# Optimization experiments

Measured on AMD Instinct MI355X. Metric: run time of the kernel, lower is better.

## Reference

```python
import jax, jax.numpy as jnp
from jax import lax
import numpy as np

STRIDE = 16
A = 9  # num anchors per location
PRE_NMS = 6000
POST_NMS = 300
NMS_THRESH = 0.7
MIN_SIZE = 16.0


def _generate_anchors(base_size=16, ratios=(0.5, 1.0, 2.0), scales=(8, 16, 32)):
    ratios = np.array(ratios, dtype=np.float64)
    scales = np.array(scales, dtype=np.float64)
    base = np.array([0, 0, base_size - 1, base_size - 1], dtype=np.float64)
    w = base[2] - base[0] + 1
    h = base[3] - base[1] + 1
    xc = base[0] + 0.5 * (w - 1)
    yc = base[1] + 0.5 * (h - 1)
    size = w * h
    ws = np.round(np.sqrt(size / ratios))
    hs = np.round(ws * ratios)
    def mk(ws, hs):
        return np.stack([xc - 0.5 * (ws - 1), yc - 0.5 * (hs - 1),
                         xc + 0.5 * (ws - 1), yc + 0.5 * (hs - 1)], axis=1)
    ratio_anchors = mk(ws, hs)  # (3,4)
    out = []
    for ra in ratio_anchors:
        rw = ra[2] - ra[0] + 1
        rh = ra[3] - ra[1] + 1
        out.append(mk(rw * scales, rh * scales))
    return np.concatenate(out, axis=0).astype(np.float32)  # (9,4)


def _conv(x, w, b, padding):
    y = lax.conv_general_dilated(x, w, (1, 1), padding,
                                 dimension_numbers=('NCHW', 'OIHW', 'NCHW'))
    return y + b[None, :, None, None]


def _rpn_forward(feature_map, im_info, conv_w, conv_b, cls_w, cls_b, bbox_w, bbox_b):
    H, W = feature_map.shape[2], feature_map.shape[3]
    x = jax.nn.relu(_conv(feature_map, conv_w, conv_b, 'SAME'))
    cls_score = _conv(x, cls_w, cls_b, 'VALID')      # [1, 2A, H, W]
    bbox_pred = _conv(x, bbox_w, bbox_b, 'VALID')    # [1, 4A, H, W]

    # softmax over the 2 classes: view (1, 2, A, H, W)
    prob = jax.nn.softmax(cls_score.reshape(1, 2, A, H, W), axis=1).reshape(1, 2 * A, H, W)
    fg_scores = prob[:, A:, :, :].transpose(0, 2, 3, 1).reshape(-1)     # [H*W*A]
    deltas = bbox_pred.transpose(0, 2, 3, 1).reshape(-1, 4)             # [H*W*A, 4]

    # anchors shifted over the grid (K, A, 4) -> (K*A, 4), x varies fastest
    base_anchors = jnp.asarray(_generate_anchors())
    shift_x = jnp.arange(W, dtype=jnp.float32) * STRIDE
    shift_y = jnp.arange(H, dtype=jnp.float32) * STRIDE
    sx, sy = jnp.meshgrid(shift_x, shift_y)  # (H, W)
    shifts = jnp.stack([sx.ravel(), sy.ravel(), sx.ravel(), sy.ravel()], axis=1)
    anchors = (base_anchors[None, :, :] + shifts[:, None, :]).reshape(-1, 4)

    # bbox_transform_inv
    aw = anchors[:, 2] - anchors[:, 0] + 1.0
    ah = anchors[:, 3] - anchors[:, 1] + 1.0
    ax = anchors[:, 0] + 0.5 * aw
    ay = anchors[:, 1] + 0.5 * ah
    dx, dy, dw, dh = deltas[:, 0], deltas[:, 1], deltas[:, 2], deltas[:, 3]
    px = dx * aw + ax
    py = dy * ah + ay
    pw = jnp.exp(dw) * aw
    ph = jnp.exp(dh) * ah
    x1 = px - 0.5 * pw
    y1 = py - 0.5 * ph
    x2 = px + 0.5 * pw
    y2 = py + 0.5 * ph

    # clip to image
    x1 = jnp.clip(x1, 0.0, im_info[1] - 1.0)
    y1 = jnp.clip(y1, 0.0, im_info[0] - 1.0)
    x2 = jnp.clip(x2, 0.0, im_info[1] - 1.0)
    y2 = jnp.clip(y2, 0.0, im_info[0] - 1.0)
    boxes = jnp.stack([x1, y1, x2, y2], axis=1)

    # min-size filter (mask instead of dropping, jit-safe)
    ws_ = x2 - x1 + 1.0
    hs_ = y2 - y1 + 1.0
    valid = (ws_ >= MIN_SIZE * im_info[2]) & (hs_ >= MIN_SIZE * im_info[2])
    scores = jnp.where(valid, fg_scores, -1e9)

    # pre-NMS top-k (descending)
    top_scores, order = lax.top_k(scores, PRE_NMS)
    top_boxes = boxes[order]  # [PRE_NMS, 4]

    # greedy NMS on sorted boxes (stop_gradient: NMS selection is non-diff)
    nb = lax.stop_gradient(top_boxes)
    areas = (nb[:, 2] - nb[:, 0] + 1.0) * (nb[:, 3] - nb[:, 1] + 1.0)
    idx = jnp.arange(PRE_NMS)

    def body(i, keep):
        xx1 = jnp.maximum(nb[i, 0], nb[:, 0])
        yy1 = jnp.maximum(nb[i, 1], nb[:, 1])
        xx2 = jnp.minimum(nb[i, 2], nb[:, 2])
        yy2 = jnp.minimum(nb[i, 3], nb[:, 3])
        inter = jnp.maximum(0.0, xx2 - xx1 + 1.0) * jnp.maximum(0.0, yy2 - yy1 + 1.0)
        iou = inter / (areas[i] + areas - inter)
        supp = (iou > NMS_THRESH) & (idx > i) & keep[i]
        return keep & ~supp

    keep = lax.fori_loop(0, PRE_NMS, body, jnp.ones(PRE_NMS, dtype=bool))

    kept_scores = jnp.where(keep, lax.stop_gradient(top_scores), -1e9)
    _, sel = lax.top_k(kept_scores, POST_NMS)  # already score-sorted, order preserved
    final_boxes = top_boxes[sel]  # [POST_NMS, 4]

    rois = jnp.concatenate([jnp.zeros((POST_NMS, 1), jnp.float32), final_boxes], axis=1)
    return rois  # [POST_NMS, 5]


def setup_inputs() -> dict:
    key = jax.random.key(0)
    ks = jax.random.split(key, 6)
    H, W, C = 100, 152, 512
    feature_map = jax.random.normal(ks[0], (1, C, H, W), jnp.float32)
    im_info = jnp.array([H * STRIDE, W * STRIDE, 1.0], jnp.float32)
    conv_w = jax.random.normal(ks[1], (C, C, 3, 3), jnp.float32) * 0.01
    conv_b = jnp.zeros((C,), jnp.float32)
    cls_w = jax.random.normal(ks[2], (2 * A, C, 1, 1), jnp.float32) * 0.01
    cls_b = jnp.zeros((2 * A,), jnp.float32)
    bbox_w = jax.random.normal(ks[3], (4 * A, C, 1, 1), jnp.float32) * 0.01
    bbox_b = jnp.zeros((4 * A,), jnp.float32)
    return {"feature_map": feature_map, "im_info": im_info,
            "conv_w": conv_w, "conv_b": conv_b,
            "cls_w": cls_w, "cls_b": cls_b,
            "bbox_w": bbox_w, "bbox_b": bbox_b}


def reference(feature_map, im_info, conv_w, conv_b, cls_w, cls_b, bbox_w, bbox_b):
    return _rpn_forward(feature_map, im_info, conv_w, conv_b, cls_w, cls_b, bbox_w, bbox_b)
```

## Files before the change

kernel.cpp:

```cpp
#include <hip/hip_runtime.h>
#include <hip/hip_bf16.h>
#include <math.h>

#define H_ 100
#define W_ 152
#define HW_ 15200
#define C_ 512
#define A_ 9
#define NA_ 136800
#define PRE_NMS_ 6000
#define NB_PAD_ 6016
#define NWORDS_ 94
#define POST_NMS_ 300

#define NCAND_ 16384
#define NBUCK_ 262144
#define SELW_  (NBUCK_ + 1024 + 16 + NCAND_ * 2)
#define SELN4_ (SELW_ / 4)

#define QH_ 102
#define QW_ 154
#define NQ_ (QH_ * QW_)

#define PX_BLOCKS_ 1968
#define PW_BLOCKS_ 1152
#define PH_BLOCKS_ 128
#define ZC_BLOCKS_ 290
#define PALL_BLOCKS_ (PX_BLOCKS_ + PW_BLOCKS_ + PH_BLOCKS_ + ZC_BLOCKS_)

typedef __attribute__((ext_vector_type(8))) short short8;
typedef __attribute__((ext_vector_type(4))) float f32x4;

#define GLOAD_LDS16(g, l) \
    __builtin_amdgcn_global_load_lds( \
        (const __attribute__((address_space(1))) void*)(g), \
        (__attribute__((address_space(3))) void*)(l), 16, 0, 0)

__global__ __launch_bounds__(256) void pack_all(
    const float* __restrict__ fm, const float* __restrict__ cw,
    const float* __restrict__ cls_w, const float* __restrict__ cls_b,
    const float* __restrict__ bbox_w, const float* __restrict__ bbox_b,
    __hip_bfloat16* __restrict__ xph, __hip_bfloat16* __restrict__ xpm,
    __hip_bfloat16* __restrict__ xpl,
    __hip_bfloat16* __restrict__ bph, __hip_bfloat16* __restrict__ bpm,
    __hip_bfloat16* __restrict__ bpl,
    float* __restrict__ wT, float* __restrict__ hb,
    unsigned* __restrict__ selbuf)
{
    __shared__ float t[64][65];
    const int tid = threadIdx.x;
    const int blk = blockIdx.x;

    if (blk < PX_BLOCKS_) {
        const int q0 = (blk % 246) * 64;
        const int c0 = (blk / 246) * 64;
        {
            const int qi = tid & 63;
            const int cs = tid >> 6;
            const int q = q0 + qi;
            int hp = q / QW_, wp = q - hp * QW_;
            bool inter = (q < NQ_) && (hp >= 1) && (hp <= 100) && (wp >= 1) && (wp <= 152);
            int p = inter ? ((hp - 1) * W_ + (wp - 1)) : 0;
#pragma unroll
            for (int cc = cs; cc < 64; cc += 4) {
                float v = inter ? fm[(size_t)(c0 + cc) * HW_ + p] : 0.f;
                t[cc][qi] = v;
            }
        }
        __syncthreads();
        {
            const int cl = tid & 63;
            const int qs = tid >> 6;
#pragma unroll
            for (int qq = qs; qq < 64; qq += 4) {
                int qg = q0 + qq;
                if (qg < NQ_) {
                    float v = t[cl][qq];
                    __hip_bfloat16 h = __float2bfloat16(v);
                    float r1 = v - __bfloat162float(h);
                    __hip_bfloat16 m = __float2bfloat16(r1);
                    float r2 = r1 - __bfloat162float(m);
                    __hip_bfloat16 l = __float2bfloat16(r2);
                    size_t o = (size_t)qg * 512 + c0 + cl;
                    xph[o] = h;
                    xpm[o] = m;
                    xpl[o] = l;
                }
            }
        }
        return;
    }
    if (blk < PX_BLOCKS_ + PW_BLOCKS_) {
        int id = (blk - PX_BLOCKS_) * 256 + tid;
        int lane = id & 63;
        int rest = id >> 6;
        int n16 = rest & 31;
        int tk = rest >> 5;
        int k32 = tk & 15;
        int t9 = tk >> 4;
        if (t9 >= 9) return;
        int ky = t9 / 3, kx = t9 - ky * 3;
        int n = n16 * 16 + (lane & 15);
        int kb = k32 * 32 + (lane >> 4) * 8;

        union H8 { short8 s; __hip_bfloat16 b[8]; } hv, mv, lv;
#pragma unroll
        for (int j = 0; j < 8; j++) {
            int ci = kb + j;
            float v = cw[(((size_t)n * 512 + ci) * 3 + ky) * 3 + kx];
            __hip_bfloat16 h = __float2bfloat16(v);
            float r1 = v - __bfloat162float(h);
            __hip_bfloat16 m = __float2bfloat16(r1);
            float r2 = r1 - __bfloat162float(m);
            hv.b[j] = h;
            mv.b[j] = m;
            lv.b[j] = __float2bfloat16(r2);
        }
        *(short8*)((short*)bph + (size_t)id * 8) = hv.s;
        *(short8*)((short*)bpm + (size_t)id * 8) = mv.s;
        *(short8*)((short*)bpl + (size_t)id * 8) = lv.s;
        return;
    }
    if (blk < PX_BLOCKS_ + PW_BLOCKS_ + PH_BLOCKS_) {
        int id = (blk - PX_BLOCKS_ - PW_BLOCKS_) * 256 + tid;
        int ci = id >> 6, c = id & 63;
        float v = 0.f;
        if (c < 18)      v = cls_w[(size_t)c * 512 + ci];
        else if (c < 54) v = bbox_w[(size_t)(c - 18) * 512 + ci];
        wT[ci * 64 + c] = v;
        if (ci == 0)
            hb[c] = (c < 18) ? cls_b[c] : (c < 54 ? bbox_b[c - 18] : 0.f);
        return;
    }
    {
        int id = (blk - PX_BLOCKS_ - PW_BLOCKS_ - PH_BLOCKS_) * 256 + tid;
        if (id < SELN4_) ((uint4*)selbuf)[id] = make_uint4(0u, 0u, 0u, 0u);
    }
}

__global__ __launch_bounds__(256, 2) void conv_mfma(
    const __hip_bfloat16* __restrict__ xph, const __hip_bfloat16* __restrict__ xpm,
    const __hip_bfloat16* __restrict__ xpl,
    const __hip_bfloat16* __restrict__ bph, const __hip_bfloat16* __restrict__ bpm,
    const __hip_bfloat16* __restrict__ bpl,
    const float* __restrict__ cb, float* __restrict__ xt)
{
    __shared__ short a_lds[24][64][8];
    __shared__ short b_lds[24][64][8];

    const int tid = threadIdx.x;
    const int wave = tid >> 6, lane = tid & 63;
    const int wm = wave >> 1, wn = wave & 1;

    const int orig = blockIdx.x;
    const int xcd  = orig & 7;
    const int idx  = orig >> 3;
    const int wgid = (xcd < 4 ? xcd * 60 : 240 + (xcd - 4) * 59) + idx;
    const int mb = wgid >> 2;
    const int nb = wgid & 3;

    const __hip_bfloat16* xarr[3] = {xph, xpm, xpl};
    const __hip_bfloat16* barr[3] = {bph, bpm, bpl};

    const int sBase = wave * 6;
    const short* aSrc[6];
    const short* bSrc[6];
#pragma unroll
    for (int i = 0; i < 6; i++) {
        int s = sBase + i;
        int f = s / 3, arr = s - 3 * (s / 3);
        int m = mb * 128 + f * 16 + (lane & 15);
        int hh = m / W_, ww = m - hh * W_;
        int q = (hh + 1) * QW_ + (ww + 1);
        aSrc[i] = (const short*)xarr[arr] + (size_t)q * 512 + (lane >> 4) * 8;
        bSrc[i] = (const short*)barr[arr] + (size_t)(nb * 8 + f) * 512 + lane * 8;
    }

    auto stage = [&](int it) {
        const int t9 = it >> 4;
        const int k32 = it & 15;
        const int t3 = t9 / 3;
        const int dy = t3 - 1, dx = t9 - t3 * 3 - 1;
        const int offA = ((dy * QW_ + dx) << 9) + (k32 << 5);
        const int offB = it << 14;
#pragma unroll
        for (int i = 0; i < 6; i++) {
            GLOAD_LDS16(aSrc[i] + offA, &a_lds[sBase + i][0][0]);
            GLOAD_LDS16(bSrc[i] + offB, &b_lds[sBase + i][0][0]);
        }
    };

    f32x4 acc[4][4];
#pragma unroll
    for (int f = 0; f < 4; f++)
#pragma unroll
        for (int g = 0; g < 4; g++)
            acc[f][g] = (f32x4){0.f, 0.f, 0.f, 0.f};

    stage(0);
    __syncthreads();

    for (int it = 0; it < 144; it++) {
        short8 ah[4], am[4], al[4], bh[4], bm[4], bl[4];
#pragma unroll
        for (int f = 0; f < 4; f++) {
            ah[f] = *(const short8*)&a_lds[(wm * 4 + f) * 3 + 0][lane][0];
            am[f] = *(const short8*)&a_lds[(wm * 4 + f) * 3 + 1][lane][0];
            al[f] = *(const short8*)&a_lds[(wm * 4 + f) * 3 + 2][lane][0];
            bh[f] = *(const short8*)&b_lds[(wn * 4 + f) * 3 + 0][lane][0];
            bm[f] = *(const short8*)&b_lds[(wn * 4 + f) * 3 + 1][lane][0];
            bl[f] = *(const short8*)&b_lds[(wn * 4 + f) * 3 + 2][lane][0];
        }
        __syncthreads();
        if (it + 1 < 144) stage(it + 1);
#pragma unroll
        for (int g = 0; g < 4; g++) {
#pragma unroll
            for (int f = 0; f < 4; f++) {
                f32x4 a = acc[f][g];
                a = __builtin_amdgcn_mfma_f32_16x16x32_bf16(ah[f], bh[g], a, 0, 0, 0);
                a = __builtin_amdgcn_mfma_f32_16x16x32_bf16(ah[f], bm[g], a, 0, 0, 0);
                a = __builtin_amdgcn_mfma_f32_16x16x32_bf16(am[f], bh[g], a, 0, 0, 0);
                a = __builtin_amdgcn_mfma_f32_16x16x32_bf16(ah[f], bl[g], a, 0, 0, 0);
                a = __builtin_amdgcn_mfma_f32_16x16x32_bf16(al[f], bh[g], a, 0, 0, 0);
                a = __builtin_amdgcn_mfma_f32_16x16x32_bf16(am[f], bm[g], a, 0, 0, 0);
                acc[f][g] = a;
            }
        }
        __syncthreads();
    }

    const int col = lane & 15, quad = lane >> 4;
#pragma unroll
    for (int g = 0; g < 4; g++) {
        int n = nb * 128 + (wn * 4 + g) * 16 + col;
        float bias = cb[n];
#pragma unroll
        for (int f = 0; f < 4; f++) {
            int m0 = mb * 128 + (wm * 4 + f) * 16 + quad * 4;
#pragma unroll
            for (int r = 0; r < 4; r++) {
                int m = m0 + r;
                if (m < HW_)
                    xt[(size_t)m * 512 + n] = fmaxf(acc[f][g][r] + bias, 0.f);
            }
        }
    }
}

__device__ const float g_bx1[9] = {-84.f,-176.f,-360.f,-56.f,-120.f,-248.f,-36.f,-80.f,-168.f};
__device__ const float g_by1[9] = {-40.f,-88.f,-184.f,-56.f,-120.f,-248.f,-80.f,-168.f,-344.f};
__device__ const float g_bx2[9] = {99.f,191.f,375.f,71.f,135.f,263.f,51.f,95.f,183.f};
__device__ const float g_by2[9] = {55.f,103.f,199.f,71.f,135.f,263.f,95.f,183.f,359.f};

__global__ __launch_bounds__(256) void rpn_head(
    const float* __restrict__ xt,
    const float* __restrict__ wT, const float* __restrict__ hb,
    const float* __restrict__ im_info,
    float* __restrict__ scores, float4* __restrict__ boxes,
    unsigned* __restrict__ cnt)
{
    __shared__ float xl[16 * 512];
    __shared__ float raw[16][56];
    const int tid = threadIdx.x;
    const int p0 = blockIdx.x * 16;

    {
        const float4* src = (const float4*)(xt + (size_t)p0 * 512);
        float4* dst = (float4*)xl;
        for (int i = tid; i < 2048; i += 256) dst[i] = src[i];
    }
    __syncthreads();

    if (tid < 216) {
        int c  = tid % 54;
        int pg = tid / 54;
        float b = hb[c];
        float a0 = b, a1 = b, a2 = b, a3 = b;
        const float* x0 = xl + (size_t)(pg * 4) * 512;
        const float* wp = wT + c;
#pragma unroll 8
        for (int ci = 0; ci < 512; ci++) {
            float wv = wp[(size_t)ci * 64];
            a0 = fmaf(wv, x0[ci], a0);
            a1 = fmaf(wv, x0[512 + ci], a1);
            a2 = fmaf(wv, x0[1024 + ci], a2);
            a3 = fmaf(wv, x0[1536 + ci], a3);
        }
        raw[pg * 4 + 0][c] = a0;
        raw[pg * 4 + 1][c] = a1;
        raw[pg * 4 + 2][c] = a2;
        raw[pg * 4 + 3][c] = a3;
    }
    __syncthreads();

    if (tid < 144) {
        int pos = tid / 9;
        int a   = tid % 9;
        int p = p0 + pos;
        int hh = p / 152;
        int ww = p - hh * 152;

        float s0 = raw[pos][a], s1 = raw[pos][9 + a];
        float fg = 1.f / (1.f + expf(s0 - s1));

        float dx = raw[pos][18 + 4 * a + 0];
        float dy = raw[pos][18 + 4 * a + 1];
        float dw = raw[pos][18 + 4 * a + 2];
        float dh = raw[pos][18 + 4 * a + 3];

        float sx = ww * 16.f, sy = hh * 16.f;
        float ax1 = g_bx1[a] + sx, ay1 = g_by1[a] + sy;
        float ax2 = g_bx2[a] + sx, ay2 = g_by2[a] + sy;
        float aw = ax2 - ax1 + 1.f, ah = ay2 - ay1 + 1.f;
        float axc = ax1 + 0.5f * aw, ayc = ay1 + 0.5f * ah;

        float px = dx * aw + axc, py = dy * ah + ayc;
        float pw = expf(dw) * aw, ph = expf(dh) * ah;
        float x1 = px - 0.5f * pw, y1 = py - 0.5f * ph;
        float x2 = px + 0.5f * pw, y2 = py + 0.5f * ph;

        float imh = im_info[0], imw = im_info[1], scl = im_info[2];
        x1 = fminf(fmaxf(x1, 0.f), imw - 1.f);
        y1 = fminf(fmaxf(y1, 0.f), imh - 1.f);
        x2 = fminf(fmaxf(x2, 0.f), imw - 1.f);
        y2 = fminf(fmaxf(y2, 0.f), imh - 1.f);

        float wd = x2 - x1 + 1.f, hd = y2 - y1 + 1.f;
        bool valid = (wd >= 16.f * scl) && (hd >= 16.f * scl);

        int idx = p * 9 + a;
        float sv = valid ? fg : -1000000000.f;
        scores[idx] = sv;
        boxes[idx] = make_float4(x1, y1, x2, y2);

        unsigned b32 = __float_as_uint(sv);
        unsigned u = (b32 & 0x80000000u) ? ~b32 : (b32 | 0x80000000u);
        atomicAdd(&cnt[u >> 14], 1u);
    }
}

__global__ __launch_bounds__(256) void seg_sum(const unsigned* __restrict__ cnt,
                                               unsigned* __restrict__ segSum)
{
    __shared__ unsigned sh[256];
    const int s = blockIdx.x;
    const int t = threadIdx.x;
    sh[t] = cnt[s * 256 + t];
    __syncthreads();
    for (int o = 128; o > 0; o >>= 1) {
        if (t < o) sh[t] += sh[t + o];
        __syncthreads();
    }
    if (t == 0) segSum[s] = sh[0];
}

__global__ __launch_bounds__(256) void find_thresh(const unsigned* __restrict__ cnt,
                                                   const unsigned* __restrict__ segSum,
                                                   unsigned* __restrict__ meta)
{
    __shared__ unsigned a[1024];
    __shared__ unsigned strip[256];
    __shared__ unsigned suf2[256];
    __shared__ int sStarSh, hStarSh;
    __shared__ unsigned cumASh;
    const int t = threadIdx.x;

    for (int i = t; i < 1024; i += 256) a[i] = segSum[i];
    if (t == 0) { sStarSh = -1; hStarSh = -1; }
    __syncthreads();

    const unsigned e0 = a[4 * t + 0], e1 = a[4 * t + 1];
    const unsigned e2 = a[4 * t + 2], e3 = a[4 * t + 3];
    const unsigned own = e0 + e1 + e2 + e3;
    strip[t] = own;
    __syncthreads();

    unsigned val = own;
    for (int o = 1; o < 256; o <<= 1) {
        unsigned w = (t + o < 256) ? strip[t + o] : 0u;
        __syncthreads();
        val += w;
        strip[t] = val;
        __syncthreads();
    }
    const unsigned sufExcl = strip[t] - own;

    unsigned si3 = sufExcl + e3;
    unsigned si2 = si3 + e2;
    unsigned si1 = si2 + e1;
    unsigned si0 = si1 + e0;
    int best = -1;
    if      (si3 >= PRE_NMS_) best = 4 * t + 3;
    else if (si2 >= PRE_NMS_) best = 4 * t + 2;
    else if (si1 >= PRE_NMS_) best = 4 * t + 1;
    else if (si0 >= PRE_NMS_) best = 4 * t + 0;
    if (best >= 0) atomicMax(&sStarSh, best);
    __syncthreads();
    const int sStar = sStarSh;
    if ((sStar >> 2) == t) {
        int r = sStar & 3;
        unsigned inc = (r == 3) ? si3 : (r == 2) ? si2 : (r == 1) ? si1 : si0;
        cumASh = inc - a[sStar];
    }
    __syncthreads();
    const unsigned cumA = cumASh;

    unsigned c = cnt[sStar * 256 + t];
    suf2[t] = c;
    __syncthreads();
    unsigned v2 = c;
    for (int o = 1; o < 256; o <<= 1) {
        unsigned w = (t + o < 256) ? suf2[t + o] : 0u;
        __syncthreads();
        v2 += w;
        suf2[t] = v2;
        __syncthreads();
    }
    if (cumA + suf2[t] >= PRE_NMS_) atomicMax(&hStarSh, t);
    __syncthreads();
    if (t == 0) {
        int hh = hStarSh;
        meta[0] = (unsigned)(sStar * 256 + hh);
        meta[1] = cumA + suf2[hh];
    }
}

__global__ __launch_bounds__(256) void compact_top(const float* __restrict__ scores,
                                                   const unsigned* __restrict__ meta,
                                                   unsigned long long* __restrict__ cand,
                                                   unsigned* __restrict__ ctr)
{
    int g = blockIdx.x * 256 + threadIdx.x;
    if (g >= NA_) return;
    unsigned hStar = meta[0];
    unsigned b = __float_as_uint(scores[g]);
    unsigned u = (b & 0x80000000u) ? ~b : (b | 0x80000000u);
    if ((u >> 14) >= hStar) {
        unsigned pos = atomicAdd(ctr, 1u);
        if (pos < (unsigned)NCAND_)
            cand[pos] = ((unsigned long long)u << 32) |
                        (unsigned long long)(0xFFFFFFFFu - (unsigned)g);
    }
}

__device__ __forceinline__ void cex(unsigned long long* s, int i, int l, bool desc)
{
    unsigned long long a = s[i], b = s[l];
    if (desc ? (a < b) : (a > b)) { s[i] = b; s[l] = a; }
}

__global__ __launch_bounds__(256) void bitonic_local_sort_keys(unsigned long long* __restrict__ keys)
{
    __shared__ unsigned long long s[4096];
    const int tid = threadIdx.x;
    const int base = blockIdx.x * 4096;
    for (int i = tid; i < 4096; i += 256) s[i] = keys[base + i];
    __syncthreads();
    for (int k = 2; k <= 4096; k <<= 1) {
        for (int j = k >> 1; j > 0; j >>= 1) {
#pragma unroll
            for (int m = 0; m < 8; m++) {
                int p = tid + m * 256;
                int i = ((p & ~(j - 1)) << 1) | (p & (j - 1));
                int l = i | j;
                bool desc = (((base + i) & k) == 0);
                cex(s, i, l, desc);
            }
            __syncthreads();
        }
    }
    for (int i = tid; i < 4096; i += 256) keys[base + i] = s[i];
}

__global__ void bitonic_global(unsigned long long* __restrict__ keys, int j, int k)
{
    int p = blockIdx.x * 256 + threadIdx.x;
    int i = ((p & ~(j - 1)) << 1) | (p & (j - 1));
    int l = i | j;
    bool desc = ((i & k) == 0);
    unsigned long long a = keys[i], b = keys[l];
    if (desc ? (a < b) : (a > b)) { keys[i] = b; keys[l] = a; }
}

__global__ __launch_bounds__(256) void bitonic_local_merge(unsigned long long* __restrict__ keys, int k)
{
    __shared__ unsigned long long s[4096];
    const int tid = threadIdx.x;
    const int base = blockIdx.x * 4096;
    const bool desc = ((base & k) == 0);
    for (int i = tid; i < 4096; i += 256) s[i] = keys[base + i];
    __syncthreads();
    for (int j = 2048; j > 0; j >>= 1) {
#pragma unroll
        for (int m = 0; m < 8; m++) {
            int p = tid + m * 256;
            int i = ((p & ~(j - 1)) << 1) | (p & (j - 1));
            cex(s, i, i | j, desc);
        }
        __syncthreads();
    }
    for (int i = tid; i < 4096; i += 256) keys[base + i] = s[i];
}

__global__ __launch_bounds__(256) void bitonic_local_merge_gather(
    unsigned long long* __restrict__ keys, int k,
    const float* __restrict__ scores, const float4* __restrict__ boxes,
    float4* __restrict__ nb, float* __restrict__ sc, float* __restrict__ area)
{
    __shared__ unsigned long long s[4096];
    const int tid = threadIdx.x;
    const int base = blockIdx.x * 4096;
    const bool desc = ((base & k) == 0);
    for (int i = tid; i < 4096; i += 256) s[i] = keys[base + i];
    __syncthreads();
    for (int j = 2048; j > 0; j >>= 1) {
#pragma unroll
        for (int m = 0; m < 8; m++) {
            int p = tid + m * 256;
            int i = ((p & ~(j - 1)) << 1) | (p & (j - 1));
            cex(s, i, i | j, desc);
        }
        __syncthreads();
    }
    for (int i = tid; i < 4096; i += 256) {
        int r = base + i;
        keys[r] = s[i];
        if (r < NB_PAD_) {
            if (r < PRE_NMS_) {
                unsigned long long key = s[i];
                unsigned idx = 0xFFFFFFFFu - (unsigned)(key & 0xFFFFFFFFull);
                float4 b = boxes[idx];
                nb[r] = b;
                sc[r] = scores[idx];
                area[r] = (b.z - b.x + 1.f) * (b.w - b.y + 1.f);
            } else {
                nb[r] = make_float4(0.f, 0.f, 0.f, 0.f);
                sc[r] = -1000000000.f;
                area[r] = 1.f;
            }
        }
    }
}

__global__ __launch_bounds__(256) void nms_mask(const float4* __restrict__ nb,
                                                const float* __restrict__ area,
                                                unsigned long long* __restrict__ mask,
                                                unsigned long long* __restrict__ diag)
{
    __shared__ float4 cbox[64];
    __shared__ float carea[64];
    const int t = threadIdx.x;
    const int cbk = blockIdx.x;
    const int rb  = blockIdx.y * 4 + (t >> 6);
    const int lane = t & 63;
    const int jBase = cbk * 64;
    if (t < 64) { cbox[t] = nb[jBase + t]; carea[t] = area[jBase + t]; }
    __syncthreads();
    if (rb >= NWORDS_) return;

    const int i = rb * 64 + lane;
    const float4 bi = nb[i];
    const float ai = area[i];
    unsigned long long bits = 0ull;
#pragma unroll 8
    for (int b = 0; b < 64; b++) {
        int j = jBase + b;
        if (j > i) {
            float4 bj = cbox[b];
            float xx1 = fmaxf(bi.x, bj.x), yy1 = fmaxf(bi.y, bj.y);
            float xx2 = fminf(bi.z, bj.z), yy2 = fminf(bi.w, bj.w);
            float iw = fmaxf(0.f, xx2 - xx1 + 1.f);
            float ih = fmaxf(0.f, yy2 - yy1 + 1.f);
            float inter = iw * ih;
            float iou = inter / (ai + carea[b] - inter);
            if (iou > 0.7f) bits |= (1ull << b);
        }
    }
    mask[(size_t)cbk * NB_PAD_ + i] = bits;
    if (cbk == rb) diag[i] = bits;
}

__device__ __forceinline__ unsigned long long readlane_u64(unsigned long long v, int l)
{
    unsigned int lo = (unsigned int)__builtin_amdgcn_readlane((int)(unsigned int)(v & 0xffffffffull), l);
    unsigned int hi = (unsigned int)__builtin_amdgcn_readlane((int)(unsigned int)(v >> 32), l);
    return ((unsigned long long)hi << 32) | (unsigned long long)lo;
}

__global__ __launch_bounds__(256) void nms_final(const unsigned long long* __restrict__ mask,
                                                 const unsigned long long* __restrict__ diag,
                                                 const float* __restrict__ sc,
                                                 const float4* __restrict__ nb,
                                                 float* __restrict__ out)
{
    __shared__ unsigned long long dlds[NB_PAD_];
    __shared__ unsigned rlo[NWORDS_], rhi[NWORDS_];
    __shared__ unsigned long long aliveW[NWORDS_];
    __shared__ unsigned long long aliveSh;
    __shared__ int sel[POST_NMS_];
    __shared__ int brkSh, keptCumSh;
    const int tid = threadIdx.x;
    const int wave = tid >> 6, lane = tid & 63;

    for (int i = tid; i < NB_PAD_; i += 256) dlds[i] = diag[i];
    if (tid < NWORDS_) { rlo[tid] = 0u; rhi[tid] = 0u; }
    if (tid == 0) { brkSh = NWORDS_; keptCumSh = 0; }
    __syncthreads();

    for (int c = 0; c < NWORDS_; c++) {
        unsigned long long ext = ((unsigned long long)rhi[c] << 32) | (unsigned long long)rlo[c];
        unsigned long long aliveP = ~ext;

        unsigned long long mysel = aliveP & (0xFFFFull << (wave * 16));
        int rb[16];
        int n = 0;
        while (mysel) { rb[n++] = (int)__builtin_ctzll(mysel); mysel &= mysel - 1; }

        unsigned long long v0[16], v1[16];
#pragma unroll
        for (int i = 0; i < 16; i++) {
            if (i < n) {
                int row = c * 64 + rb[i];
                v0[i] = mask[(size_t)lane * NB_PAD_ + row];
                v1[i] = (lane < NWORDS_ - 64)
                          ? mask[(size_t)(64 + lane) * NB_PAD_ + row] : 0ull;
            }
        }

        if (wave == 0) {
            unsigned long long myD = dlds[c * 64 + lane];
            unsigned long long alive = aliveP, todo = aliveP;
            while (todo) {
                int l = (int)__builtin_ctzll(todo);
                todo &= todo - 1;
                unsigned long long d = readlane_u64(myD, l);
                alive &= ~d;
                todo &= ~d;
            }
            bool vld = sc[c * 64 + lane] > -5e8f;
            unsigned long long vb = __ballot(vld);
            if (lane == 0) {
                aliveSh = alive;
                aliveW[c] = alive;
                keptCumSh += __popcll(alive & vb);
                if (keptCumSh >= POST_NMS_ && brkSh == NWORDS_) brkSh = c;
            }
        }
        __syncthreads();

        if (brkSh <= c) break;

        unsigned long long alive = aliveSh;
        unsigned long long d0 = 0ull, d1 = 0ull;
#pragma unroll
        for (int i = 0; i < 16; i++) {
            if (i < n && ((alive >> rb[i]) & 1ull)) { d0 |= v0[i]; d1 |= v1[i]; }
        }
        if (d0) {
            atomicOr(&rlo[lane], (unsigned)d0);
            atomicOr(&rhi[lane], (unsigned)(d0 >> 32));
        }
        if (lane < NWORDS_ - 64 && d1) {
            atomicOr(&rlo[64 + lane], (unsigned)d1);
            atomicOr(&rhi[64 + lane], (unsigned)(d1 >> 32));
        }
        __syncthreads();
    }

    if (wave == 0) {
        const unsigned long long lmask = (lane == 0) ? 0ull : ((~0ull) >> (64 - lane));
        int cntk = 0;
        for (int c = 0; c < NWORDS_ && cntk < POST_NMS_; c++) {
            int j = c * 64 + lane;
            bool k = (j < PRE_NMS_) && (((aliveW[c] >> lane) & 1ull) != 0ull) && (sc[j] > -5e8f);
            unsigned long long bal = __ballot(k);
            int pos = cntk + __popcll(bal & lmask);
            if (k && pos < POST_NMS_) sel[pos] = j;
            cntk += __popcll(bal);
        }
        if (cntk < POST_NMS_) {
            for (int c = 0; c < NWORDS_ && cntk < POST_NMS_; c++) {
                int j = c * 64 + lane;
                bool k = (j < PRE_NMS_) && !((((aliveW[c] >> lane) & 1ull) != 0ull) && (sc[j] > -5e8f));
                unsigned long long bal = __ballot(k);
                int pos = cntk + __popcll(bal & lmask);
                if (k && pos < POST_NMS_) sel[pos] = j;
                cntk += __popcll(bal);
            }
        }
    }
    __syncthreads();
    for (int i = tid; i < POST_NMS_; i += 256) {
        int j = sel[i];
        float4 b = nb[j];
        out[i * 5 + 0] = 0.f;
        out[i * 5 + 1] = b.x;
        out[i * 5 + 2] = b.y;
        out[i * 5 + 3] = b.z;
        out[i * 5 + 4] = b.w;
    }
}

extern "C" void kernel_launch(void* const* d_in, const int* in_sizes, int n_in,
                              void* d_out, int out_size, void* d_ws, size_t ws_size,
                              hipStream_t stream)
{
    const float* fm      = (const float*)d_in[0];
    const float* im_info = (const float*)d_in[1];
    const float* conv_w  = (const float*)d_in[2];
    const float* conv_b  = (const float*)d_in[3];
    const float* cls_w   = (const float*)d_in[4];
    const float* cls_b   = (const float*)d_in[5];
    const float* bbox_w  = (const float*)d_in[6];
    const float* bbox_b  = (const float*)d_in[7];
    float* out = (float*)d_out;

    char* ws = (char*)d_ws;
    size_t off = 0;
    auto alloc = [&](size_t bytes) -> void* {
        void* p = ws + off;
        off = (off + bytes + 255) & ~(size_t)255;
        return p;
    };
    float* xt    = (float*)alloc((size_t)HW_ * 512 * 4);
    float* wT    = (float*)alloc((size_t)512 * 64 * 4);
    float* hb    = (float*)alloc(64 * 4);
    unsigned* selbuf = (unsigned*)alloc((size_t)SELW_ * 4);
    unsigned* cnt    = selbuf;
    unsigned* segSum = selbuf + NBUCK_;
    unsigned* meta   = selbuf + NBUCK_ + 1024;
    unsigned long long* cand = (unsigned long long*)(selbuf + NBUCK_ + 1024 + 16);

    size_t phase_base = off;
    __hip_bfloat16* xph = (__hip_bfloat16*)alloc((size_t)NQ_ * 512 * 2);
    __hip_bfloat16* xpm = (__hip_bfloat16*)alloc((size_t)NQ_ * 512 * 2);
    __hip_bfloat16* xpl = (__hip_bfloat16*)alloc((size_t)NQ_ * 512 * 2);
    __hip_bfloat16* bph = (__hip_bfloat16*)alloc((size_t)9 * 512 * 512 * 2);
    __hip_bfloat16* bpm = (__hip_bfloat16*)alloc((size_t)9 * 512 * 512 * 2);
    __hip_bfloat16* bpl = (__hip_bfloat16*)alloc((size_t)9 * 512 * 512 * 2);

    off = phase_base;
    float* scores             = (float*)alloc((size_t)NA_ * 4);
    float4* boxes             = (float4*)alloc((size_t)NA_ * 16);
    float4* nb                = (float4*)alloc((size_t)NB_PAD_ * 16);
    float* sc                 = (float*)alloc((size_t)NB_PAD_ * 4);
    float* area               = (float*)alloc((size_t)NB_PAD_ * 4);
    unsigned long long* mask  = (unsigned long long*)alloc((size_t)NB_PAD_ * NWORDS_ * 8);
    unsigned long long* diag  = (unsigned long long*)alloc((size_t)NB_PAD_ * 8);

    pack_all<<<dim3(PALL_BLOCKS_), 256, 0, stream>>>(
        fm, conv_w, cls_w, cls_b, bbox_w, bbox_b,
        xph, xpm, xpl, bph, bpm, bpl, wT, hb, selbuf);
    conv_mfma<<<dim3(476), 256, 0, stream>>>(xph, xpm, xpl, bph, bpm, bpl,
                                             conv_b, xt);
    rpn_head<<<dim3(950), 256, 0, stream>>>(xt, wT, hb, im_info, scores, boxes, cnt);
    seg_sum<<<dim3(1024), 256, 0, stream>>>(cnt, segSum);
    find_thresh<<<dim3(1), 256, 0, stream>>>(cnt, segSum, meta);
    compact_top<<<dim3((NA_ + 255) / 256), 256, 0, stream>>>(scores, meta, cand,
                                                             meta + 2);
    bitonic_local_sort_keys<<<dim3(4), 256, 0, stream>>>(cand);
    bitonic_global<<<dim3(32), 256, 0, stream>>>(cand, 4096, 8192);
    bitonic_local_merge<<<dim3(4), 256, 0, stream>>>(cand, 8192);
    bitonic_global<<<dim3(32), 256, 0, stream>>>(cand, 8192, 16384);
    bitonic_global<<<dim3(32), 256, 0, stream>>>(cand, 4096, 16384);
    bitonic_local_merge_gather<<<dim3(4), 256, 0, stream>>>(cand, 16384,
                                                            scores, boxes,
                                                            nb, sc, area);
    nms_mask<<<dim3(NWORDS_, 24), 256, 0, stream>>>(nb, area, mask, diag);
    nms_final<<<dim3(1), 256, 0, stream>>>(mask, diag, sc, nb, out);
}
```

Measured before the change: 759.0 us.

## Fold segment sums into find_thresh, use 8K-wide local bitonic sort, skip lower-triangle NMS blocks

Removes the separate seg_sum kernel by having find_thresh reduce the histogram itself with wave shuffles. The candidate sort now uses 8192-key shared-memory blocks, which cuts the launch chain from six kernels to three. nms_mask also exits early for column blocks below the row block, since only the upper triangle is used. The cost is less parallelism: one block now does the whole histogram reduction and two blocks do the local sorts, each using 64KB of LDS, and nms_final must never read the skipped mask words.

```diff
diff --git a/kernel.cpp b/kernel.cpp
--- a/kernel.cpp
+++ b/kernel.cpp
@@ -15,7 +15,7 @@
 
 #define NCAND_ 16384
 #define NBUCK_ 262144
-#define SELW_  (NBUCK_ + 1024 + 16 + NCAND_ * 2)
+#define SELW_  (NBUCK_ + 16 + NCAND_ * 2)
 #define SELN4_ (SELW_ / 4)
 
 #define QH_ 102
@@ -25,7 +25,7 @@
 #define PX_BLOCKS_ 1968
 #define PW_BLOCKS_ 1152
 #define PH_BLOCKS_ 128
-#define ZC_BLOCKS_ 290
+#define ZC_BLOCKS_ 289
 #define PALL_BLOCKS_ (PX_BLOCKS_ + PW_BLOCKS_ + PH_BLOCKS_ + ZC_BLOCKS_)
 
 typedef __attribute__((ext_vector_type(8))) short short8;
@@ -340,23 +340,7 @@
     }
 }
 
-__global__ __launch_bounds__(256) void seg_sum(const unsigned* __restrict__ cnt,
-                                               unsigned* __restrict__ segSum)
-{
-    __shared__ unsigned sh[256];
-    const int s = blockIdx.x;
-    const int t = threadIdx.x;
-    sh[t] = cnt[s * 256 + t];
-    __syncthreads();
-    for (int o = 128; o > 0; o >>= 1) {
-        if (t < o) sh[t] += sh[t + o];
-        __syncthreads();
-    }
-    if (t == 0) segSum[s] = sh[0];
-}
-
 __global__ __launch_bounds__(256) void find_thresh(const unsigned* __restrict__ cnt,
-                                                   const unsigned* __restrict__ segSum,
                                                    unsigned* __restrict__ meta)
 {
     __shared__ unsigned a[1024];
@@ -365,8 +349,16 @@
     __shared__ int sStarSh, hStarSh;
     __shared__ unsigned cumASh;
     const int t = threadIdx.x;
-
-    for (int i = t; i < 1024; i += 256) a[i] = segSum[i];
+    const int wave = t >> 6, lane = t & 63;
+
+    for (int s = wave; s < 1024; s += 4) {
+        unsigned v = 0;
+#pragma unroll
+        for (int r = 0; r < 4; ++r) v += cnt[s * 256 + lane + r * 64];
+#pragma unroll
+        for (int o = 32; o > 0; o >>= 1) v += __shfl_down(v, o);
+        if (lane == 0) a[s] = v;
+    }
     if (t == 0) { sStarSh = -1; hStarSh = -1; }
     __syncthreads();
 
@@ -450,17 +442,17 @@
     if (desc ? (a < b) : (a > b)) { s[i] = b; s[l] = a; }
 }
 
-__global__ __launch_bounds__(256) void bitonic_local_sort_keys(unsigned long long* __restrict__ keys)
-{
-    __shared__ unsigned long long s[4096];
+__global__ __launch_bounds__(256) void bitonic_local_sort8k(unsigned long long* __restrict__ keys)
+{
+    __shared__ unsigned long long s[8192];
     const int tid = threadIdx.x;
-    const int base = blockIdx.x * 4096;
-    for (int i = tid; i < 4096; i += 256) s[i] = keys[base + i];
-    __syncthreads();
-    for (int k = 2; k <= 4096; k <<= 1) {
+    const int base = blockIdx.x * 8192;
+    for (int i = tid; i < 8192; i += 256) s[i] = keys[base + i];
+    __syncthreads();
+    for (int k = 2; k <= 8192; k <<= 1) {
         for (int j = k >> 1; j > 0; j >>= 1) {
 #pragma unroll
-            for (int m = 0; m < 8; m++) {
+            for (int m = 0; m < 16; m++) {
                 int p = tid + m * 256;
                 int i = ((p & ~(j - 1)) << 1) | (p & (j - 1));
                 int l = i | j;
@@ -470,7 +462,7 @@
             __syncthreads();
         }
     }
-    for (int i = tid; i < 4096; i += 256) keys[base + i] = s[i];
+    for (int i = tid; i < 8192; i += 256) keys[base + i] = s[i];
 }
 
 __global__ void bitonic_global(unsigned long long* __restrict__ keys, int j, int k)
@@ -483,49 +475,27 @@
     if (desc ? (a < b) : (a > b)) { keys[i] = b; keys[l] = a; }
 }
 
-__global__ __launch_bounds__(256) void bitonic_local_merge(unsigned long long* __restrict__ keys, int k)
-{
-    __shared__ unsigned long long s[4096];
+__global__ __launch_bounds__(256) void bitonic_merge8k_gather(
+    const unsigned long long* __restrict__ keys,
+    const float* __restrict__ scores, const float4* __restrict__ boxes,
+    float4* __restrict__ nb, float* __restrict__ sc, float* __restrict__ area)
+{
+    __shared__ unsigned long long s[8192];
     const int tid = threadIdx.x;
-    const int base = blockIdx.x * 4096;
-    const bool desc = ((base & k) == 0);
-    for (int i = tid; i < 4096; i += 256) s[i] = keys[base + i];
-    __syncthreads();
-    for (int j = 2048; j > 0; j >>= 1) {
-#pragma unroll
-        for (int m = 0; m < 8; m++) {
+    const int base = blockIdx.x * 8192;
+    for (int i = tid; i < 8192; i += 256) s[i] = keys[base + i];
+    __syncthreads();
+    for (int j = 4096; j > 0; j >>= 1) {
+#pragma unroll
+        for (int m = 0; m < 16; m++) {
             int p = tid + m * 256;
             int i = ((p & ~(j - 1)) << 1) | (p & (j - 1));
-            cex(s, i, i | j, desc);
-        }
-        __syncthreads();
-    }
-    for (int i = tid; i < 4096; i += 256) keys[base + i] = s[i];
-}
-
-__global__ __launch_bounds__(256) void bitonic_local_merge_gather(
-    unsigned long long* __restrict__ keys, int k,
-    const float* __restrict__ scores, const float4* __restrict__ boxes,
-    float4* __restrict__ nb, float* __restrict__ sc, float* __restrict__ area)
-{
-    __shared__ unsigned long long s[4096];
-    const int tid = threadIdx.x;
-    const int base = blockIdx.x * 4096;
-    const bool desc = ((base & k) == 0);
-    for (int i = tid; i < 4096; i += 256) s[i] = keys[base + i];
-    __syncthreads();
-    for (int j = 2048; j > 0; j >>= 1) {
-#pragma unroll
-        for (int m = 0; m < 8; m++) {
-            int p = tid + m * 256;
-            int i = ((p & ~(j - 1)) << 1) | (p & (j - 1));
-            cex(s, i, i | j, desc);
-        }
-        __syncthreads();
-    }
-    for (int i = tid; i < 4096; i += 256) {
+            cex(s, i, i | j, true);
+        }
+        __syncthreads();
+    }
+    for (int i = tid; i < 8192; i += 256) {
         int r = base + i;
-        keys[r] = s[i];
         if (r < NB_PAD_) {
             if (r < PRE_NMS_) {
                 unsigned long long key = s[i];
@@ -557,7 +527,7 @@
     const int jBase = cbk * 64;
     if (t < 64) { cbox[t] = nb[jBase + t]; carea[t] = area[jBase + t]; }
     __syncthreads();
-    if (rb >= NWORDS_) return;
+    if (rb >= NWORDS_ || cbk < rb) return;
 
     const int i = rb * 64 + lane;
     const float4 bi = nb[i];
@@ -728,9 +698,8 @@
     float* hb    = (float*)alloc(64 * 4);
     unsigned* selbuf = (unsigned*)alloc((size_t)SELW_ * 4);
     unsigned* cnt    = selbuf;
-    unsigned* segSum = selbuf + NBUCK_;
-    unsigned* meta   = selbuf + NBUCK_ + 1024;
-    unsigned long long* cand = (unsigned long long*)(selbuf + NBUCK_ + 1024 + 16);
+    unsigned* meta   = selbuf + NBUCK_;
+    unsigned long long* cand = (unsigned long long*)(selbuf + NBUCK_ + 16);
 
     size_t phase_base = off;
     __hip_bfloat16* xph = (__hip_bfloat16*)alloc((size_t)NQ_ * 512 * 2);
@@ -755,18 +724,13 @@
     conv_mfma<<<dim3(476), 256, 0, stream>>>(xph, xpm, xpl, bph, bpm, bpl,
                                              conv_b, xt);
     rpn_head<<<dim3(950), 256, 0, stream>>>(xt, wT, hb, im_info, scores, boxes, cnt);
-    seg_sum<<<dim3(1024), 256, 0, stream>>>(cnt, segSum);
-    find_thresh<<<dim3(1), 256, 0, stream>>>(cnt, segSum, meta);
+    find_thresh<<<dim3(1), 256, 0, stream>>>(cnt, meta);
     compact_top<<<dim3((NA_ + 255) / 256), 256, 0, stream>>>(scores, meta, cand,
                                                              meta + 2);
-    bitonic_local_sort_keys<<<dim3(4), 256, 0, stream>>>(cand);
-    bitonic_global<<<dim3(32), 256, 0, stream>>>(cand, 4096, 8192);
-    bitonic_local_merge<<<dim3(4), 256, 0, stream>>>(cand, 8192);
+    bitonic_local_sort8k<<<dim3(2), 256, 0, stream>>>(cand);
     bitonic_global<<<dim3(32), 256, 0, stream>>>(cand, 8192, 16384);
-    bitonic_global<<<dim3(32), 256, 0, stream>>>(cand, 4096, 16384);
-    bitonic_local_merge_gather<<<dim3(4), 256, 0, stream>>>(cand, 16384,
-                                                            scores, boxes,
-                                                            nb, sc, area);
+    bitonic_merge8k_gather<<<dim3(2), 256, 0, stream>>>(cand, scores, boxes,
+                                                        nb, sc, area);
     nms_mask<<<dim3(NWORDS_, 24), 256, 0, stream>>>(nb, area, mask, diag);
     nms_final<<<dim3(1), 256, 0, stream>>>(mask, diag, sc, nb, out);
 }
```

Result: slower. 958.7 us (+26.3%).
